# Kernel optimization log

Measured on AMD Instinct MI355X. Metric: run time of the kernel, lower is better.

## Reference

```python
import jax, jax.numpy as jnp
import numpy as np

B, P, ENC = 64, 196, 512
EMB = ATT = DEC = 256
V = 10000
T = 44


def setup_inputs() -> dict:
    key = jax.random.key(0)
    ks = jax.random.split(key, 16)
    def xavier(k, shape):
        fan_out, fan_in = shape
        std = (2.0 / (fan_in + fan_out)) ** 0.5
        return jax.random.normal(k, shape, dtype=jnp.float32) * std
    return {
        "encoder_out": jax.random.normal(ks[0], (B, P, ENC), dtype=jnp.float32),
        "caption": jax.random.randint(ks[1], (B, T), 0, V),
        "W_enc_att": xavier(ks[2], (ATT, ENC)),
        "W_dec_att": xavier(ks[3], (ATT, DEC)),
        "W_full": xavier(ks[4], (1, ATT)),
        "embedding": jax.random.normal(ks[5], (V, EMB), dtype=jnp.float32) * 0.02,
        "W_init_h": xavier(ks[6], (DEC, ENC)),
        "b_init_h": jnp.zeros((DEC,), dtype=jnp.float32),
        "W_init_c": xavier(ks[7], (DEC, ENC)),
        "b_init_c": jnp.zeros((DEC,), dtype=jnp.float32),
        "W_ih": jax.random.normal(ks[8], (4 * DEC, EMB + ENC), dtype=jnp.float32) * 0.03,
        "b_ih": jnp.zeros((4 * DEC,), dtype=jnp.float32),
        "W_hh": jax.random.normal(ks[9], (4 * DEC, DEC), dtype=jnp.float32) * 0.03,
        "b_hh": jnp.zeros((4 * DEC,), dtype=jnp.float32),
        "W_out": xavier(ks[10], (V, DEC)),
        "b_out": jnp.zeros((V,), dtype=jnp.float32),
    }


def _decoder(encoder_out, caption, W_enc_att, W_dec_att, W_full, embedding,
             W_init_h, b_init_h, W_init_c, b_init_c,
             W_ih, b_ih, W_hh, b_hh, W_out, b_out):
    # embeddings: [B, T, EMB] -> time-major [T, B, EMB]
    emb = embedding[caption].transpose(1, 0, 2)
    # init hidden state from mean pooled encoder features
    avg = encoder_out.mean(axis=1)                      # [B, ENC]
    h0 = avg @ W_init_h.T + b_init_h                    # [B, DEC]
    c0 = avg @ W_init_c.T + b_init_c
    # attention key projection of encoder, constant over time
    att1 = jnp.einsum('bpe,ae->bpa', encoder_out, W_enc_att)  # [B, P, ATT]

    def step(carry, emb_t):
        h, c = carry
        # additive attention
        att2 = h @ W_dec_att.T                          # [B, ATT]
        scores = jnp.einsum('bpa,a->bp',
                            jax.nn.relu(att1 + att2[:, None, :]), W_full[0])
        alpha = jax.nn.softmax(scores, axis=1)          # [B, P]
        ctx = jnp.einsum('bp,bpe->be', alpha, encoder_out)  # [B, ENC]
        # LSTM cell (torch gate order: i, f, g, o)
        x = jnp.concatenate([ctx, emb_t], axis=1)       # [B, ENC+EMB]
        gates = x @ W_ih.T + b_ih + h @ W_hh.T + b_hh   # [B, 4*DEC]
        i, f, g, o = jnp.split(gates, 4, axis=1)
        c_new = jax.nn.sigmoid(f) * c + jax.nn.sigmoid(i) * jnp.tanh(g)
        h_new = jax.nn.sigmoid(o) * jnp.tanh(c_new)
        logits = h_new @ W_out.T + b_out                # [B, V]
        return (h_new, c_new), (logits, alpha)

    # NOTE: torch cat order is [weighted_context, embedding]
    (_, _), (logits, alphas) = jax.lax.scan(step, (h0, c0), emb)
    predictions = logits.transpose(1, 0, 2)             # [B, T, V]
    alphas = alphas.transpose(1, 0, 2)                  # [B, T, P]
    return predictions, alphas


def reference(encoder_out, caption, W_enc_att, W_dec_att, W_full, embedding,
              W_init_h, b_init_h, W_init_c, b_init_c,
              W_ih, b_ih, W_hh, b_hh, W_out, b_out):
    return _decoder(encoder_out, caption, W_enc_att, W_dec_att, W_full, embedding,
                    W_init_h, b_init_h, W_init_c, b_init_c,
                    W_ih, b_ih, W_hh, b_hh, W_out, b_out)
```

## Files before the change

kernel.cpp:

```cpp
#include <hip/hip_runtime.h>

#define B_   64
#define P_   196
#define ENC_ 512
#define ATT_ 256
#define DEC_ 256
#define EMB_ 256
#define V_   10000
#define T_   44
#define G4_  1024
#define XW_  768
#define A1N_ 26624

using short8 = __attribute__((ext_vector_type(8))) short;
using f32x4  = __attribute__((ext_vector_type(4))) float;
typedef _Float16 f16x2 __attribute__((ext_vector_type(2)));

__device__ __forceinline__ unsigned short f2bf(float f) {
    unsigned int u = __float_as_uint(f);
    unsigned int r = (u + 0x7fffu + ((u >> 16) & 1u)) >> 16;
    return (unsigned short)r;
}

__device__ __forceinline__ unsigned int pkh2(float a, float b) {
    f16x2 t; t.x = (_Float16)a; t.y = (_Float16)b;
    return __builtin_bit_cast(unsigned int, t);
}

__device__ __forceinline__ float fdot2f(float wbits, f16x2 xv, float acc) {
    f16x2 wv = __builtin_bit_cast(f16x2, wbits);
#if __has_builtin(__builtin_amdgcn_fdot2)
    return __builtin_amdgcn_fdot2(wv, xv, acc, false);
#else
    acc = fmaf((float)wv.x, (float)xv.x, acc);
    acc = fmaf((float)wv.y, (float)xv.y, acc);
    return acc;
#endif
}
__device__ __forceinline__ float fdot2u(unsigned int wbits, f16x2 xv, float acc) {
    f16x2 wv = __builtin_bit_cast(f16x2, wbits);
#if __has_builtin(__builtin_amdgcn_fdot2)
    return __builtin_amdgcn_fdot2(wv, xv, acc, false);
#else
    acc = fmaf((float)wv.x, (float)xv.x, acc);
    acc = fmaf((float)wv.y, (float)xv.y, acc);
    return acc;
#endif
}

__device__ __forceinline__ void bar() {
    asm volatile("s_waitcnt lgkmcnt(0)" ::: "memory");
    __builtin_amdgcn_s_barrier();
    asm volatile("" ::: "memory");
}

__global__ void k_transpose(const float* __restrict__ src, float* __restrict__ dst,
                            int N, int stride, int off) {
    __shared__ float t[32][33];
    int k0 = blockIdx.x * 32, n0 = blockIdx.y * 32;
    int tx = threadIdx.x & 31, ty = threadIdx.x >> 5;
    for (int r = ty; r < 32; r += 8)
        t[r][tx] = src[(size_t)(n0 + r) * stride + off + k0 + tx];
    __syncthreads();
    for (int r = ty; r < 32; r += 8)
        dst[(size_t)(k0 + r) * N + n0 + tx] = t[tx][r];
}

__global__ __launch_bounds__(256) void k_packWda(const float* __restrict__ Wda,
                                                 float4* __restrict__ WdaP4) {
    int d4 = blockIdx.x, a = threadIdx.x;
    float4 v;
    v.x = Wda[(size_t)a * DEC_ + 4 * d4 + 0];
    v.y = Wda[(size_t)a * DEC_ + 4 * d4 + 1];
    v.z = Wda[(size_t)a * DEC_ + 4 * d4 + 2];
    v.w = Wda[(size_t)a * DEC_ + 4 * d4 + 3];
    WdaP4[(size_t)d4 * 256 + a] = v;
}

__global__ __launch_bounds__(256) void k_packWg(const float* __restrict__ Wih,
        const float* __restrict__ Whh, float4* __restrict__ Wg4) {
    int k2 = blockIdx.x, d = threadIdx.x;
    int k = 2 * k2;
    unsigned int o[4];
#pragma unroll
    for (int g = 0; g < 4; ++g) {
        int row = g * 256 + d;
        float a0, a1;
        if (k < ENC_) {
            a0 = Wih[(size_t)row * XW_ + k];
            a1 = Wih[(size_t)row * XW_ + k + 1];
        } else {
            a0 = Whh[(size_t)row * DEC_ + k - ENC_];
            a1 = Whh[(size_t)row * DEC_ + k - ENC_ + 1];
        }
        o[g] = pkh2(a0, a1);
    }
    float4 v;
    v.x = __builtin_bit_cast(float, o[0]);
    v.y = __builtin_bit_cast(float, o[1]);
    v.z = __builtin_bit_cast(float, o[2]);
    v.w = __builtin_bit_cast(float, o[3]);
    Wg4[(size_t)k2 * 256 + d] = v;
}

__global__ __launch_bounds__(256) void k_packenc(const float* __restrict__ enc,
                                                 uint2* __restrict__ encPh) {
    int b = blockIdx.x, p4b = blockIdx.y * 7;
    for (int p4 = p4b; p4 < p4b + 7; ++p4) {
        for (int e = threadIdx.x; e < ENC_; e += 256) {
            float a0 = enc[((size_t)b * P_ + 4 * p4 + 0) * ENC_ + e];
            float a1 = enc[((size_t)b * P_ + 4 * p4 + 1) * ENC_ + e];
            float a2 = enc[((size_t)b * P_ + 4 * p4 + 2) * ENC_ + e];
            float a3 = enc[((size_t)b * P_ + 4 * p4 + 3) * ENC_ + e];
            uint2 v; v.x = pkh2(a0, a1); v.y = pkh2(a2, a3);
            encPh[((size_t)b * 49 + p4) * ENC_ + e] = v;
        }
    }
}

__global__ void k_cvt(const float* __restrict__ src, unsigned short* __restrict__ dst, int n) {
    int i = blockIdx.x * 256 + threadIdx.x;
    if (i < n) dst[i] = f2bf(src[i]);
}

__global__ __launch_bounds__(256) void k_init_state(
        const float* __restrict__ enc,
        const float* __restrict__ W_init_h, const float* __restrict__ b_init_h,
        const float* __restrict__ W_init_c, const float* __restrict__ b_init_c,
        float* __restrict__ h0, float* __restrict__ c0) {
    int b = blockIdx.x, tid = threadIdx.x;
    __shared__ float avg[ENC_];
    for (int e = tid; e < ENC_; e += 256) {
        float s = 0.f;
        const float* p = enc + (size_t)b * P_ * ENC_ + e;
        for (int i = 0; i < P_; i++) s += p[(size_t)i * ENC_];
        avg[e] = s * (1.0f / (float)P_);
    }
    __syncthreads();
    int d = tid;
    float hs = b_init_h[d], cs = b_init_c[d];
    const float* wh = W_init_h + (size_t)d * ENC_;
    const float* wc = W_init_c + (size_t)d * ENC_;
    for (int e = 0; e < ENC_; e++) { float a = avg[e]; hs += a * wh[e]; cs += a * wc[e]; }
    h0[b * DEC_ + d] = hs;
    c0[b * DEC_ + d] = cs;
}

__global__ __launch_bounds__(256) void k_att1(
        const float* __restrict__ enc, const float* __restrict__ Wea,
        unsigned int* __restrict__ att1h) {
    int b = blockIdx.x >> 2, a0 = (blockIdx.x & 3) * 64;
    __shared__ float encT[32][257];
    __shared__ float Wt[64][32];
    int tid = threadIdx.x;
    int pl = tid & 63, ia = tid >> 6;
    float acc[16][4];
#pragma unroll
    for (int k = 0; k < 16; k++)
#pragma unroll
        for (int qq = 0; qq < 4; qq++) acc[k][qq] = 0.f;

    for (int e0 = 0; e0 < ENC_; e0 += 32) {
        {
            int j = tid & 31, pr = tid >> 5;
            for (int pass = 0; pass < 32; pass++) {
                int p = pr + pass * 8;
                float v = 0.f;
                if (p < P_) v = enc[((size_t)b * P_ + p) * ENC_ + e0 + j];
                encT[j][p] = v;
            }
            int r = tid >> 2, c0 = (tid & 3) * 8;
#pragma unroll
            for (int i = 0; i < 8; i++)
                Wt[r][c0 + i] = Wea[(size_t)(a0 + r) * ENC_ + e0 + c0 + i];
        }
        __syncthreads();
        for (int e = 0; e < 32; e++) {
            float e0v = encT[e][pl], e1v = encT[e][pl + 64];
            float e2v = encT[e][pl + 128], e3v = encT[e][pl + 192];
#pragma unroll
            for (int k = 0; k < 16; k++) {
                float w = Wt[ia * 16 + k][e];
                acc[k][0] += w * e0v; acc[k][1] += w * e1v;
                acc[k][2] += w * e2v; acc[k][3] += w * e3v;
            }
        }
        __syncthreads();
    }
#pragma unroll
    for (int k = 0; k < 16; k += 2)
#pragma unroll
        for (int qq = 0; qq < 4; qq++) {
            int p = pl + 64 * qq;
            int a = a0 + ia * 16 + k;
            if (p < P_)
                att1h[(size_t)b * A1N_ + (size_t)(a >> 1) * 208 + p] =
                    pkh2(acc[k][qq], acc[k + 1][qq]);
        }
}

__global__ __launch_bounds__(256) void k_embW(
        const int* __restrict__ caption, const float* __restrict__ embedding,
        const float* __restrict__ WiheT, const float* __restrict__ b_ih,
        const float* __restrict__ b_hh, float* __restrict__ embW) {
    int r0 = blockIdx.x * 16, tid = threadIdx.x;
    __shared__ float embL[16][256];
    __shared__ int capL[16];
    if (tid < 16) {
        int r = r0 + tid, t = r >> 6, b = r & 63;
        capL[tid] = caption[b * T_ + t];
    }
    __syncthreads();
#pragma unroll
    for (int lr = 0; lr < 16; lr++)
        embL[lr][tid] = embedding[(size_t)capL[lr] * EMB_ + tid];
    __syncthreads();
    float base0 = b_ih[tid] + b_hh[tid];
    float base1 = b_ih[tid + 256] + b_hh[tid + 256];
    float base2 = b_ih[tid + 512] + b_hh[tid + 512];
    float base3 = b_ih[tid + 768] + b_hh[tid + 768];
    float acc[16][4];
#pragma unroll
    for (int lr = 0; lr < 16; lr++) {
        acc[lr][0] = base0; acc[lr][1] = base1; acc[lr][2] = base2; acc[lr][3] = base3;
    }
    for (int e = 0; e < EMB_; e++) {
        const float* wr = WiheT + (size_t)e * G4_ + tid;
        float w0 = wr[0], w1 = wr[256], w2 = wr[512], w3 = wr[768];
#pragma unroll
        for (int lr = 0; lr < 16; lr++) {
            float ev = embL[lr][e];
            acc[lr][0] += w0 * ev; acc[lr][1] += w1 * ev;
            acc[lr][2] += w2 * ev; acc[lr][3] += w3 * ev;
        }
    }
#pragma unroll
    for (int lr = 0; lr < 16; lr++) {
        float* o = embW + (size_t)(r0 + lr) * G4_ + tid;
        o[0] = acc[lr][0]; o[256] = acc[lr][1]; o[512] = acc[lr][2]; o[768] = acc[lr][3];
    }
}

__global__ __launch_bounds__(1024, 4) void k_recur(
        const unsigned int* __restrict__ att1h, const float4* __restrict__ WdaP4,
        const float* __restrict__ W_full, const float4* __restrict__ Wg4,
        const float* __restrict__ embW, const uint2* __restrict__ encPh,
        const float* __restrict__ h0, const float* __restrict__ c0,
        unsigned short* __restrict__ Hbf, float* __restrict__ out_alpha) {
    int b = blockIdx.x, tid = threadIdx.x;
    int q = tid >> 8;
    int r = tid & 255;
    int e5 = tid & 511, ph = tid >> 9;

    __shared__ __align__(16) float h_l[DEC_];
    __shared__ __align__(16) float att2_l[ATT_];
    __shared__ __align__(16) float wf_l[ATT_];
    __shared__ __align__(16) _Float16 xh[XW_];
    __shared__ float p1[4][256];
    __shared__ float p2[4][256];
    __shared__ float p3[2][512];
    __shared__ __align__(16) float4 p4s[4][256];
    __shared__ float red_l[4];
    __shared__ __align__(8) _Float16 alpha_h[208];
    __shared__ unsigned int att1_lds[A1N_ + 48];

    {
        const unsigned int* a1g = att1h + (size_t)b * A1N_;
        for (int i = tid; i < A1N_; i += 1024) att1_lds[i] = a1g[i];
    }
    if (tid < 256) {
        float hv = h0[b * DEC_ + tid];
        h_l[tid] = hv;
        xh[512 + tid] = (_Float16)hv;
        wf_l[tid] = W_full[tid];
    }
    float c = (tid < 256) ? c0[b * DEC_ + tid] : 0.f;
    __syncthreads();

    const uint2* encb = encPh + (size_t)b * (49 * ENC_);

    for (int t = 0; t < T_; ++t) {
        float a2 = 0.f;
#pragma unroll 4
        for (int i = 0; i < 16; i++) {
            int d4 = q * 16 + i;
            float4 w = WdaP4[(size_t)d4 * 256 + r];
            float4 h4 = *reinterpret_cast<const float4*>(&h_l[4 * d4]);
            a2 += w.x * h4.x + w.y * h4.y + w.z * h4.z + w.w * h4.w;
        }
        p1[q][r] = a2;
        bar();
        if (tid < 256) att2_l[tid] = p1[0][tid] + p1[1][tid] + p1[2][tid] + p1[3][tid];
        bar();

        float sp = 0.f;
#pragma unroll 4
        for (int i = 0; i < 32; i++) {
            int a2i = q * 32 + i;
            f16x2 av = __builtin_bit_cast(f16x2, att1_lds[a2i * 208 + r]);
            float2 t2 = *reinterpret_cast<const float2*>(&att2_l[2 * a2i]);
            float2 w4 = *reinterpret_cast<const float2*>(&wf_l[2 * a2i]);
            sp += fmaxf((float)av.x + t2.x, 0.f) * w4.x +
                  fmaxf((float)av.y + t2.y, 0.f) * w4.y;
        }
        p2[q][r] = sp;
        bar();

        float ex = 0.f;
        if (tid < 256) {
            float s = p2[0][tid] + p2[1][tid] + p2[2][tid] + p2[3][tid];
            ex = (tid < P_) ? __expf(s) : 0.f;
            float sm = ex;
#pragma unroll
            for (int off = 32; off; off >>= 1) sm += __shfl_xor(sm, off);
            if ((tid & 63) == 0) red_l[tid >> 6] = sm;
        }
        bar();
        if (tid < 256) {
            float sm = red_l[0] + red_l[1] + red_l[2] + red_l[3];
            float alpha = ex / sm;
            if (tid < 208) alpha_h[tid] = (_Float16)alpha;
            if (tid < P_) out_alpha[(size_t)b * (T_ * P_) + t * P_ + tid] = alpha;
        }
        bar();

        float cx = 0.f;
        {
            int p4b = ph ? 25 : 0, p4e = ph ? 49 : 25;
#pragma unroll 5
            for (int p4 = p4b; p4 < p4e; p4++) {
                uint2 ev = encb[(size_t)p4 * ENC_ + e5];
                f16x2 a01 = *reinterpret_cast<const f16x2*>(&alpha_h[4 * p4]);
                f16x2 a23 = *reinterpret_cast<const f16x2*>(&alpha_h[4 * p4 + 2]);
                cx = fdot2u(ev.x, a01, cx);
                cx = fdot2u(ev.y, a23, cx);
            }
        }
        p3[ph][e5] = cx;
        float ew0 = 0.f, ew1 = 0.f, ew2 = 0.f, ew3 = 0.f;
        if (tid < 256) {
            const float* ew = embW + ((size_t)t * B_ + b) * G4_;
            ew0 = ew[tid]; ew1 = ew[tid + 256]; ew2 = ew[tid + 512]; ew3 = ew[tid + 768];
        }
        bar();
        if (tid < 512) xh[tid] = (_Float16)(p3[0][tid] + p3[1][tid]);
        bar();

        float4 acc = {0.f, 0.f, 0.f, 0.f};
#pragma unroll 8
        for (int i = 0; i < 96; i++) {
            int k2 = q * 96 + i;
            float4 w = Wg4[(size_t)k2 * 256 + r];
            f16x2 xv = *reinterpret_cast<const f16x2*>(&xh[2 * k2]);
            acc.x = fdot2f(w.x, xv, acc.x);
            acc.y = fdot2f(w.y, xv, acc.y);
            acc.z = fdot2f(w.z, xv, acc.z);
            acc.w = fdot2f(w.w, xv, acc.w);
        }
        p4s[q][r] = acc;
        bar();

        if (tid < 256) {
            float4 g0 = p4s[0][tid], g1 = p4s[1][tid], g2 = p4s[2][tid], g3 = p4s[3][tid];
            float gi = g0.x + g1.x + g2.x + g3.x + ew0;
            float gf = g0.y + g1.y + g2.y + g3.y + ew1;
            float gg = g0.z + g1.z + g2.z + g3.z + ew2;
            float go = g0.w + g1.w + g2.w + g3.w + ew3;
            float i_g = 1.f / (1.f + __expf(-gi));
            float f_g = 1.f / (1.f + __expf(-gf));
            float g_g = tanhf(gg);
            float o_g = 1.f / (1.f + __expf(-go));
            c = f_g * c + i_g * g_g;
            float hn = o_g * tanhf(c);
            h_l[tid] = hn;
            xh[512 + tid] = (_Float16)hn;
            Hbf[((size_t)t * B_ + b) * DEC_ + tid] = f2bf(hn);
        }
        bar();
    }
}

__global__ __launch_bounds__(256) void k_logits(
        const unsigned short* __restrict__ Hbf, const unsigned short* __restrict__ Woutbf,
        const float* __restrict__ b_out, float* __restrict__ out) {
    int n0 = blockIdx.x * 128, m0 = blockIdx.y * 128;
    __shared__ __align__(16) unsigned short At[128][40];
    __shared__ __align__(16) unsigned short Bt[128][40];
    int tid = threadIdx.x;
    int lane = tid & 63, w = tid >> 6;
    int wm = (w & 1) * 64, wn = (w >> 1) * 64;
    f32x4 acc[4][4];
#pragma unroll
    for (int i = 0; i < 4; i++)
#pragma unroll
        for (int j = 0; j < 4; j++) acc[i][j] = (f32x4){0.f, 0.f, 0.f, 0.f};

    for (int k0 = 0; k0 < DEC_; k0 += 32) {
#pragma unroll
        for (int l = 0; l < 2; l++) {
            int idx = l * 256 + tid;
            int r = idx >> 2, kc = (idx & 3) * 8;
            uint4 av = *reinterpret_cast<const uint4*>(&Hbf[(size_t)(m0 + r) * DEC_ + k0 + kc]);
            *reinterpret_cast<uint4*>(&At[r][kc]) = av;
            uint4 bv = make_uint4(0u, 0u, 0u, 0u);
            if (n0 + r < V_)
                bv = *reinterpret_cast<const uint4*>(&Woutbf[(size_t)(n0 + r) * DEC_ + k0 + kc]);
            *reinterpret_cast<uint4*>(&Bt[r][kc]) = bv;
        }
        __syncthreads();
        int qk = (lane >> 4) * 8, fr = lane & 15;
        short8 a[4], bb[4];
#pragma unroll
        for (int i = 0; i < 4; i++) {
            a[i]  = *reinterpret_cast<const short8*>(&At[wm + i * 16 + fr][qk]);
            bb[i] = *reinterpret_cast<const short8*>(&Bt[wn + i * 16 + fr][qk]);
        }
#pragma unroll
        for (int i = 0; i < 4; i++)
#pragma unroll
            for (int j = 0; j < 4; j++)
                acc[i][j] = __builtin_amdgcn_mfma_f32_16x16x32_bf16(a[i], bb[j], acc[i][j], 0, 0, 0);
        __syncthreads();
    }
    int col = lane & 15, qr = (lane >> 4) * 4;
#pragma unroll
    for (int j = 0; j < 4; j++) {
        int n = n0 + wn + j * 16 + col;
        if (n < V_) {
            float bo = b_out[n];
#pragma unroll
            for (int i = 0; i < 4; i++)
#pragma unroll
                for (int rr = 0; rr < 4; rr++) {
                    int m = m0 + wm + i * 16 + qr + rr;
                    int t = m >> 6, bb2 = m & 63;
                    out[(size_t)bb2 * (T_ * V_) + (size_t)t * V_ + n] = acc[i][j][rr] + bo;
                }
        }
    }
}

extern "C" void kernel_launch(void* const* d_in, const int* in_sizes, int n_in,
                              void* d_out, int out_size, void* d_ws, size_t ws_size,
                              hipStream_t stream) {
    const float* enc       = (const float*)d_in[0];
    const int*   caption   = (const int*)d_in[1];
    const float* W_enc_att = (const float*)d_in[2];
    const float* W_dec_att = (const float*)d_in[3];
    const float* W_full    = (const float*)d_in[4];
    const float* embedding = (const float*)d_in[5];
    const float* W_init_h  = (const float*)d_in[6];
    const float* b_init_h  = (const float*)d_in[7];
    const float* W_init_c  = (const float*)d_in[8];
    const float* b_init_c  = (const float*)d_in[9];
    const float* W_ih      = (const float*)d_in[10];
    const float* b_ih      = (const float*)d_in[11];
    const float* W_hh      = (const float*)d_in[12];
    const float* b_hh      = (const float*)d_in[13];
    const float* W_out     = (const float*)d_in[14];
    const float* b_out     = (const float*)d_in[15];

    float* ws = (float*)d_ws;
    float* h0    = ws;
    float* c0    = ws + 16384;
    float* WdaP  = ws + 32768;
    float* WiheT = ws + 98304;
    float* Wg4   = ws + 360448;
    float* embW  = ws + 753664;
    float* att1h = ws + 3637248;
    float* encPh = ws + 5341184;
    unsigned short* Hbf    = (unsigned short*)(ws + 8552448);
    unsigned short* Woutbf = (unsigned short*)(ws + 8912896);

    float* out_pred  = (float*)d_out;
    float* out_alpha = out_pred + (size_t)B_ * T_ * V_;

    k_transpose<<<dim3(8, 32), 256, 0, stream>>>(W_ih, WiheT, G4_, XW_, ENC_);
    k_packWda<<<64, 256, 0, stream>>>(W_dec_att, (float4*)WdaP);
    k_packWg<<<384, 256, 0, stream>>>(W_ih, W_hh, (float4*)Wg4);
    k_packenc<<<dim3(64, 7), 256, 0, stream>>>(enc, (uint2*)encPh);
    k_cvt<<<10000, 256, 0, stream>>>(W_out, Woutbf, V_ * DEC_);
    k_init_state<<<B_, 256, 0, stream>>>(enc, W_init_h, b_init_h, W_init_c, b_init_c, h0, c0);
    k_att1<<<B_ * 4, 256, 0, stream>>>(enc, W_enc_att, (unsigned int*)att1h);
    k_embW<<<176, 256, 0, stream>>>(caption, embedding, WiheT, b_ih, b_hh, embW);
    k_recur<<<B_, 1024, 0, stream>>>((const unsigned int*)att1h, (const float4*)WdaP, W_full,
                                     (const float4*)Wg4, embW, (const uint2*)encPh,
                                     h0, c0, Hbf, out_alpha);
    k_logits<<<dim3(79, 22), 256, 0, stream>>>(Hbf, Woutbf, b_out, out_pred);
}
```

Measured before the change: 1.414 ms.

## Use MFMA for att1 projection, keep att1 in registers, prefetch gate weights

Rewrites the att1 precompute kernel as an fp16 MFMA GEMM tiled 128x128 per block, replacing the scalar fp32 FMA loop. The recurrent kernel now holds each thread's 32 att1 values in registers instead of staging about 104KB of att1 in LDS. It also computes the softmax denominator redundantly in every wavefront, which removes one barrier per step. A first slice of gate weights is prefetched before the barrier so the loads overlap. Freeing LDS may let more blocks fit per CU, at the cost of extra registers and fp16 rounding of the encoder inputs to att1.

```diff
diff --git a/kernel.cpp b/kernel.cpp
--- a/kernel.cpp
+++ b/kernel.cpp
@@ -13,6 +13,7 @@
 #define A1N_ 26624
 
 using short8 = __attribute__((ext_vector_type(8))) short;
+using half8  = __attribute__((ext_vector_type(8))) _Float16;
 using f32x4  = __attribute__((ext_vector_type(4))) float;
 typedef _Float16 f16x2 __attribute__((ext_vector_type(2)));
 
@@ -149,54 +150,72 @@
 __global__ __launch_bounds__(256) void k_att1(
         const float* __restrict__ enc, const float* __restrict__ Wea,
         unsigned int* __restrict__ att1h) {
-    int b = blockIdx.x >> 2, a0 = (blockIdx.x & 3) * 64;
-    __shared__ float encT[32][257];
-    __shared__ float Wt[64][32];
+    int n0 = blockIdx.x * 128;
+    int m0 = blockIdx.y * 128;
+    int b  = blockIdx.z;
+    __shared__ __align__(16) unsigned short At[128][40];
+    __shared__ __align__(16) unsigned short Bt[128][40];
     int tid = threadIdx.x;
-    int pl = tid & 63, ia = tid >> 6;
-    float acc[16][4];
-#pragma unroll
-    for (int k = 0; k < 16; k++)
-#pragma unroll
-        for (int qq = 0; qq < 4; qq++) acc[k][qq] = 0.f;
-
-    for (int e0 = 0; e0 < ENC_; e0 += 32) {
-        {
-            int j = tid & 31, pr = tid >> 5;
-            for (int pass = 0; pass < 32; pass++) {
-                int p = pr + pass * 8;
-                float v = 0.f;
-                if (p < P_) v = enc[((size_t)b * P_ + p) * ENC_ + e0 + j];
-                encT[j][p] = v;
+    int lane = tid & 63, w = tid >> 6;
+    int wm = (w & 1) * 64, wn = (w >> 1) * 64;
+    f32x4 acc[4][4];
+#pragma unroll
+    for (int i = 0; i < 4; i++)
+#pragma unroll
+        for (int j = 0; j < 4; j++) acc[i][j] = (f32x4){0.f, 0.f, 0.f, 0.f};
+
+    for (int k0 = 0; k0 < ENC_; k0 += 32) {
+#pragma unroll
+        for (int l = 0; l < 2; l++) {
+            int idx = l * 256 + tid;
+            int r = idx >> 2, kc = (idx & 3) * 8;
+            const float* ap = Wea + (size_t)(m0 + r) * ENC_ + k0 + kc;
+            float4 f0 = *reinterpret_cast<const float4*>(ap);
+            float4 f1 = *reinterpret_cast<const float4*>(ap + 4);
+            uint4 av;
+            av.x = pkh2(f0.x, f0.y); av.y = pkh2(f0.z, f0.w);
+            av.z = pkh2(f1.x, f1.y); av.w = pkh2(f1.z, f1.w);
+            *reinterpret_cast<uint4*>(&At[r][kc]) = av;
+            uint4 bv = make_uint4(0u, 0u, 0u, 0u);
+            int p = n0 + r;
+            if (p < P_) {
+                const float* bp = enc + ((size_t)b * P_ + p) * ENC_ + k0 + kc;
+                float4 g0 = *reinterpret_cast<const float4*>(bp);
+                float4 g1 = *reinterpret_cast<const float4*>(bp + 4);
+                bv.x = pkh2(g0.x, g0.y); bv.y = pkh2(g0.z, g0.w);
+                bv.z = pkh2(g1.x, g1.y); bv.w = pkh2(g1.z, g1.w);
             }
-            int r = tid >> 2, c0 = (tid & 3) * 8;
-#pragma unroll
-            for (int i = 0; i < 8; i++)
-                Wt[r][c0 + i] = Wea[(size_t)(a0 + r) * ENC_ + e0 + c0 + i];
+            *reinterpret_cast<uint4*>(&Bt[r][kc]) = bv;
         }
         __syncthreads();
-        for (int e = 0; e < 32; e++) {
-            float e0v = encT[e][pl], e1v = encT[e][pl + 64];
-            float e2v = encT[e][pl + 128], e3v = encT[e][pl + 192];
-#pragma unroll
-            for (int k = 0; k < 16; k++) {
-                float w = Wt[ia * 16 + k][e];
-                acc[k][0] += w * e0v; acc[k][1] += w * e1v;
-                acc[k][2] += w * e2v; acc[k][3] += w * e3v;
+        int qk = (lane >> 4) * 8, fr = lane & 15;
+        half8 a[4], bb[4];
+#pragma unroll
+        for (int i = 0; i < 4; i++) {
+            a[i]  = *reinterpret_cast<const half8*>(&At[wm + i * 16 + fr][qk]);
+            bb[i] = *reinterpret_cast<const half8*>(&Bt[wn + i * 16 + fr][qk]);
+        }
+#pragma unroll
+        for (int i = 0; i < 4; i++)
+#pragma unroll
+            for (int j = 0; j < 4; j++)
+                acc[i][j] = __builtin_amdgcn_mfma_f32_16x16x32_f16(a[i], bb[j], acc[i][j], 0, 0, 0);
+        __syncthreads();
+    }
+    unsigned int* eb = att1h + (size_t)b * A1N_;
+    int col = lane & 15, qr = (lane >> 4) * 4;
+#pragma unroll
+    for (int j = 0; j < 4; j++) {
+        int p = n0 + wn + j * 16 + col;
+        if (p < 208) {
+#pragma unroll
+            for (int i = 0; i < 4; i++) {
+                int a0r = m0 + wm + i * 16 + qr;
+                eb[(size_t)(a0r >> 1) * 208 + p]       = pkh2(acc[i][j][0], acc[i][j][1]);
+                eb[(size_t)((a0r >> 1) + 1) * 208 + p] = pkh2(acc[i][j][2], acc[i][j][3]);
             }
         }
-        __syncthreads();
-    }
-#pragma unroll
-    for (int k = 0; k < 16; k += 2)
-#pragma unroll
-        for (int qq = 0; qq < 4; qq++) {
-            int p = pl + 64 * qq;
-            int a = a0 + ia * 16 + k;
-            if (p < P_)
-                att1h[(size_t)b * A1N_ + (size_t)(a >> 1) * 208 + p] =
-                    pkh2(acc[k][qq], acc[k + 1][qq]);
-        }
+    }
 }
 
 __global__ __launch_bounds__(256) void k_embW(
@@ -256,17 +275,18 @@
     __shared__ __align__(16) float att2_l[ATT_];
     __shared__ __align__(16) float wf_l[ATT_];
     __shared__ __align__(16) _Float16 xh[XW_];
+    __shared__ __align__(8)  _Float16 alpha_h[208];
     __shared__ float p1[4][256];
     __shared__ float p2[4][256];
     __shared__ float p3[2][512];
     __shared__ __align__(16) float4 p4s[4][256];
-    __shared__ float red_l[4];
-    __shared__ __align__(8) _Float16 alpha_h[208];
-    __shared__ unsigned int att1_lds[A1N_ + 48];
-
+
+    unsigned int a1r[32];
     {
-        const unsigned int* a1g = att1h + (size_t)b * A1N_;
-        for (int i = tid; i < A1N_; i += 1024) att1_lds[i] = a1g[i];
+        int rc = (r < 208) ? r : 207;
+        const unsigned int* a1g = att1h + (size_t)b * A1N_ + (size_t)(q * 32) * 208 + rc;
+#pragma unroll
+        for (int i = 0; i < 32; i++) a1r[i] = a1g[(size_t)i * 208];
     }
     if (tid < 256) {
         float hv = h0[b * DEC_ + tid];
@@ -294,31 +314,37 @@
         bar();
 
         float sp = 0.f;
-#pragma unroll 4
+#pragma unroll
         for (int i = 0; i < 32; i++) {
             int a2i = q * 32 + i;
-            f16x2 av = __builtin_bit_cast(f16x2, att1_lds[a2i * 208 + r]);
+            f16x2 av = __builtin_bit_cast(f16x2, a1r[i]);
             float2 t2 = *reinterpret_cast<const float2*>(&att2_l[2 * a2i]);
             float2 w4 = *reinterpret_cast<const float2*>(&wf_l[2 * a2i]);
             sp += fmaxf((float)av.x + t2.x, 0.f) * w4.x +
                   fmaxf((float)av.y + t2.y, 0.f) * w4.y;
         }
         p2[q][r] = sp;
-        bar();
-
-        float ex = 0.f;
+        float4 gPre[6];
+#pragma unroll
+        for (int i = 0; i < 6; i++) gPre[i] = Wg4[(size_t)(q * 96 + i) * 256 + r];
+        bar();
+
+        float sden = 0.f;
+        {
+            int l = tid & 63;
+#pragma unroll
+            for (int cq = 0; cq < 4; cq++) {
+                int cc = l + cq * 64;
+                float s = p2[0][cc] + p2[1][cc] + p2[2][cc] + p2[3][cc];
+                sden += (cc < P_) ? __expf(s) : 0.f;
+            }
+#pragma unroll
+            for (int off = 32; off; off >>= 1) sden += __shfl_xor(sden, off);
+        }
         if (tid < 256) {
             float s = p2[0][tid] + p2[1][tid] + p2[2][tid] + p2[3][tid];
-            ex = (tid < P_) ? __expf(s) : 0.f;
-            float sm = ex;
-#pragma unroll
-            for (int off = 32; off; off >>= 1) sm += __shfl_xor(sm, off);
-            if ((tid & 63) == 0) red_l[tid >> 6] = sm;
-        }
-        bar();
-        if (tid < 256) {
-            float sm = red_l[0] + red_l[1] + red_l[2] + red_l[3];
-            float alpha = ex / sm;
+            float ex = (tid < P_) ? __expf(s) : 0.f;
+            float alpha = ex / sden;
             if (tid < 208) alpha_h[tid] = (_Float16)alpha;
             if (tid < P_) out_alpha[(size_t)b * (T_ * P_) + t * P_ + tid] = alpha;
         }
@@ -347,8 +373,17 @@
         bar();
 
         float4 acc = {0.f, 0.f, 0.f, 0.f};
-#pragma unroll 8
-        for (int i = 0; i < 96; i++) {
+#pragma unroll
+        for (int i = 0; i < 6; i++) {
+            int k2 = q * 96 + i;
+            f16x2 xv = *reinterpret_cast<const f16x2*>(&xh[2 * k2]);
+            acc.x = fdot2f(gPre[i].x, xv, acc.x);
+            acc.y = fdot2f(gPre[i].y, xv, acc.y);
+            acc.z = fdot2f(gPre[i].z, xv, acc.z);
+            acc.w = fdot2f(gPre[i].w, xv, acc.w);
+        }
+#pragma unroll 6
+        for (int i = 6; i < 96; i++) {
             int k2 = q * 96 + i;
             float4 w = Wg4[(size_t)k2 * 256 + r];
             f16x2 xv = *reinterpret_cast<const f16x2*>(&xh[2 * k2]);
@@ -481,7 +516,7 @@
     k_packenc<<<dim3(64, 7), 256, 0, stream>>>(enc, (uint2*)encPh);
     k_cvt<<<10000, 256, 0, stream>>>(W_out, Woutbf, V_ * DEC_);
     k_init_state<<<B_, 256, 0, stream>>>(enc, W_init_h, b_init_h, W_init_c, b_init_c, h0, c0);
-    k_att1<<<B_ * 4, 256, 0, stream>>>(enc, W_enc_att, (unsigned int*)att1h);
+    k_att1<<<dim3(2, 2, 64), 256, 0, stream>>>(enc, W_enc_att, (unsigned int*)att1h);
     k_embW<<<176, 256, 0, stream>>>(caption, embedding, WiheT, b_ih, b_hh, embW);
     k_recur<<<B_, 1024, 0, stream>>>((const unsigned int*)att1h, (const float4*)WdaP, W_full,
                                      (const float4*)Wg4, embW, (const uint2*)encPh,
```

New measurement: 2.115 ms. 1.5x slower.
